# Kernel optimization log

Hardware: AMD Instinct MI355X
Metric: run time of the kernel (lower is better)

Reference implementation:

```python
import jax, jax.numpy as jnp
import numpy as np

NINF = -1e5  # large negative used for forbidden transitions (as in partial-tagger)


def setup_inputs() -> dict:
    key = jax.random.key(0)
    ks = jax.random.split(key, 10)
    B, T, H, N = 64, 512, 768, 25
    embeddings = jax.random.normal(ks[0], (B, T, H), jnp.float32)
    lengths = jax.random.randint(ks[1], (B,), T // 2, T + 1)
    mask = jnp.arange(T)[None, :] < lengths[:, None]  # [B,T] bool
    W = jax.random.normal(ks[2], (H, N), jnp.float32) / np.sqrt(H).astype(np.float32)
    b = jnp.zeros((N,), jnp.float32)
    transitions = jax.random.normal(ks[3], (N, N), jnp.float32) * 0.1
    start_transitions = jax.random.normal(ks[4], (N,), jnp.float32) * 0.1
    end_transitions = jax.random.normal(ks[5], (N,), jnp.float32) * 0.1
    start_constraints = (jax.random.uniform(ks[6], (N,)) < 0.7).at[0].set(True)
    end_constraints = (jax.random.uniform(ks[7], (N,)) < 0.7).at[0].set(True)
    transition_constraints = (jax.random.uniform(ks[8], (N, N)) < 0.6) | jnp.eye(N, dtype=bool)
    return dict(embeddings=embeddings, W=W, b=b, transitions=transitions,
                start_transitions=start_transitions, end_transitions=end_transitions,
                mask=mask, start_constraints=start_constraints, end_constraints=end_constraints,
                transition_constraints=transition_constraints, padding_index=0)


def _log_potentials(embeddings, W, b, transitions, start_transitions, end_transitions, mask):
    # emissions [B,T,N]; lp[b,t,k,j] = emit[b,t,j] + trans[k,j]
    B, T, _ = embeddings.shape
    N = transitions.shape[0]
    logits = jnp.einsum('bth,hn->btn', embeddings, W) + b
    lp = logits[:, :, None, :] + transitions[None, None]  # [B,T,N,N]
    first = jnp.broadcast_to((start_transitions + logits[:, 0])[:, None, :], (B, N, N))
    lp = lp.at[:, 0].set(first)
    last_pos = mask.sum(-1) - 1  # [B]
    end_mask = jnp.arange(T)[None, :] == last_pos[:, None]  # [B,T]
    lp = lp + jnp.where(end_mask[:, :, None, None], end_transitions[None, None, None, :], 0.0)
    return lp


def _constrain(lp, mask, start_constraints, end_constraints, transition_constraints):
    B, T, N, _ = lp.shape
    tc = jnp.where(transition_constraints, 0.0, NINF)  # [N,N]
    sc = jnp.where(start_constraints, 0.0, NINF)       # [N]
    ec = jnp.where(end_constraints, 0.0, NINF)         # [N]
    clp = lp + tc[None, None]
    clp = clp.at[:, 0].set(lp[:, 0] + sc[None, None, :])  # start constraint, no transition constraint at t=0
    last_pos = mask.sum(-1) - 1
    end_mask = jnp.arange(T)[None, :] == last_pos[:, None]
    clp = clp + jnp.where(end_mask[:, :, None, None], ec[None, None, None, :], 0.0)
    # padded steps: force a 0-score self transition so they don't affect the path score
    eye = jnp.where(jnp.eye(N, dtype=bool), 0.0, NINF)
    clp = jnp.where(mask[:, :, None, None], clp, eye[None, None])
    return clp


def _viterbi(clp):
    # clp: [B,T,N,N] constrained log potentials -> best tag sequence [B,T]
    clp_t = jnp.swapaxes(clp, 0, 1)  # time-major [T,B,N,N]
    alpha0 = clp_t[0, :, 0, :]  # first-step rows are identical -> take row 0, [B,N]

    def fwd_step(alpha, lp_t):
        scores = alpha[:, :, None] + lp_t  # [B,N,N]
        return jnp.max(scores, axis=1), jnp.argmax(scores, axis=1).astype(jnp.int32)

    alpha_T, backptrs = jax.lax.scan(fwd_step, alpha0, clp_t[1:])  # backptrs [T-1,B,N]
    last_tag = jnp.argmax(alpha_T, axis=-1).astype(jnp.int32)  # [B]

    def bwd_step(tag, bp):
        prev = jnp.take_along_axis(bp, tag[:, None], axis=1).squeeze(1)
        return prev, prev

    _, prevs = jax.lax.scan(bwd_step, last_tag, backptrs, reverse=True)  # [T-1,B]
    tags = jnp.concatenate([prevs, last_tag[None]], axis=0).T  # [B,T]
    return tags


def reference(embeddings, W, b, transitions, start_transitions, end_transitions,
              mask, start_constraints, end_constraints, transition_constraints, padding_index):
    lp = _log_potentials(embeddings, W, b, transitions, start_transitions, end_transitions, mask)
    clp = _constrain(lp, mask, start_constraints, end_constraints, transition_constraints)
    tags = _viterbi(clp)
    out_tags = tags * mask + padding_index * (~mask)
    return lp, out_tags
```

## Files before the change

### kernel.cpp

```cpp
#include <hip/hip_runtime.h>
#include <hip/hip_bf16.h>
#include <stdint.h>

#define NINF -100000.0f

constexpr int Bn = 64, Tn = 512, Hn = 768, Nn = 25;

typedef float float2v __attribute__((ext_vector_type(2)));

__device__ inline float2v pk_mul(float2v a, float2v b) {
    float2v d;
    asm("v_pk_mul_f32 %0, %1, %2" : "=v"(d) : "v"(a), "v"(b));
    return d;
}
__device__ inline float2v pk_add(float2v a, float2v b) {
    float2v d;
    asm("v_pk_add_f32 %0, %1, %2" : "=v"(d) : "v"(a), "v"(b));
    return d;
}

__device__ inline float ldf(const void* p, size_t i, bool isbf) {
    if (isbf) return __bfloat162float(((const __hip_bfloat16*)p)[i]);
    return ((const float*)p)[i];
}
__device__ inline int ldb(const void* p, int i, int bw) {
    if (bw == 1) return (int)((const uint8_t*)p)[i];
    if (bw == 8) return ((const int*)p)[2 * i];
    return ((const int*)p)[i];
}

__device__ inline float rdlane(float v, int lane) {
    return __int_as_float(__builtin_amdgcn_readlane(__float_as_int(v), lane));
}
__device__ inline int imin2(int a, int b) { return a < b ? a : b; }

__device__ inline float amax25(const float* s) {
    float a0 = fmaxf(fmaxf(s[0],  s[1]),  s[2]);
    float a1 = fmaxf(fmaxf(s[3],  s[4]),  s[5]);
    float a2 = fmaxf(fmaxf(s[6],  s[7]),  s[8]);
    float a3 = fmaxf(fmaxf(s[9],  s[10]), s[11]);
    float a4 = fmaxf(fmaxf(s[12], s[13]), s[14]);
    float a5 = fmaxf(fmaxf(s[15], s[16]), s[17]);
    float a6 = fmaxf(fmaxf(s[18], s[19]), s[20]);
    float a7 = fmaxf(fmaxf(s[21], s[22]), s[23]);
    float b0 = fmaxf(fmaxf(a0, a1), a2);
    float b1 = fmaxf(fmaxf(a3, a4), a5);
    float b2 = fmaxf(fmaxf(a6, a7), s[24]);
    return fmaxf(fmaxf(b0, b1), b2);
}

__device__ inline float stepx(float areg, float Lg, const float* ttc) {
    float s[25];
    {
#pragma clang fp contract(off)
#pragma unroll
        for (int k = 0; k < 25; k++) {
            float ak = rdlane(areg, k);
            s[k] = ak + (Lg + ttc[k]);
        }
    }
    return amax25(s);
}

__global__ __launch_bounds__(128) void k_front(
    const void* embv, const void* mask, const void* padidx,
    const void* W, const void* bv, const void* trans, const void* startt, const void* endt,
    const void* sc, const void* ec, const void* tc,
    int* flags, float* wstrans, float* wstc,
    float* wsstart, float* wsend, float* wsscm, float* wsecm,
    int* lengths, float* logitsF)
{
    __shared__ float etile[64][76];
    __shared__ float wtile[64][32];
    __shared__ float s_b[25];
    __shared__ int   s_isbf;
    __shared__ int   ws2[2];

    int tid = threadIdx.x;
    int bid = blockIdx.x;

    if (tid < 64) {
        const uint16_t* e16 = (const uint16_t*)embv;
        uint16_t v = e16[tid];
        int ex = (v >> 7) & 0xFF;
        bool sane = (ex >= 100 && ex <= 140);
        unsigned long long ball = __ballot(sane);
        if (tid == 0) s_isbf = (__popcll(ball) >= 56) ? 1 : 0;
    }
    __syncthreads();
    bool isbf = s_isbf != 0;

    if (bid >= 512) {
        int pb = bid - 512;
        const int* mw = (const int*)mask;
        int w0 = mw[0], w1 = mw[1];
        int bw;
        if ((unsigned)w0 > 1u) bw = 1;
        else if (w0 == 1 && w1 == 0) bw = 8;
        else bw = 4;
        if (pb == 0 && tid == 0) {
            flags[0] = isbf ? 1 : 0;
            flags[1] = bw;
            flags[2] = ((const int*)padidx)[0];
        }
        {
            int s = 0;
#pragma unroll
            for (int u = 0; u < 4; u++)
                s += (ldb(mask, pb * Tn + u * 128 + tid, bw) ? 1 : 0);
            for (int off = 32; off; off >>= 1) s += __shfl_down(s, off, 64);
            if ((tid & 63) == 0) ws2[tid >> 6] = s;
            __syncthreads();
            if (tid == 0) lengths[pb] = ws2[0] + ws2[1];
        }
        int gid = pb * 128 + tid;
        int gsz = 64 * 128;
        for (int i = gid; i < Nn; i += gsz) {
            wsstart[i] = ldf(startt, i, isbf);
            wsend[i]   = ldf(endt, i, isbf);
            wsscm[i]   = ldb(sc, i, bw) ? 0.0f : NINF;
            wsecm[i]   = ldb(ec, i, bw) ? 0.0f : NINF;
        }
        for (int i = gid; i < Nn * Nn; i += gsz) {
            wstrans[i] = ldf(trans, i, isbf);
            wstc[i]    = ldb(tc, i, bw) ? 0.0f : NINF;
        }
        return;
    }

    int r    = tid >> 1;
    int half = tid & 1;
    int j0   = half ? 12 : 0;
    int row0 = bid * 64;
    int row  = row0 + r;

    if (tid < 25) s_b[tid] = ldf(bv, tid, isbf);

    float2v acc2[6];
#pragma unroll
    for (int k = 0; k < 6; k++) acc2[k] = (float2v){0.0f, 0.0f};
    float acc12 = 0.0f;

    for (int c = 0; c < 12; c++) {
        __syncthreads();
        if (isbf) {
            const uint16_t* ep = (const uint16_t*)embv;
#pragma unroll
            for (int it = 0; it < 8; it++) {
                int idx = it * 128 + tid;
                int rr = idx >> 4;
                int q  = idx & 15;
                const ushort4* p4 = (const ushort4*)(ep + (size_t)(row0 + rr) * Hn + c * 64);
                ushort4 u = p4[q];
                float4 f;
                f.x = __bfloat162float(*(const __hip_bfloat16*)&u.x);
                f.y = __bfloat162float(*(const __hip_bfloat16*)&u.y);
                f.z = __bfloat162float(*(const __hip_bfloat16*)&u.z);
                f.w = __bfloat162float(*(const __hip_bfloat16*)&u.w);
                *(float4*)&etile[rr][q * 4] = f;
            }
        } else {
            const float* ep = (const float*)embv;
#pragma unroll
            for (int it = 0; it < 8; it++) {
                int idx = it * 128 + tid;
                int rr = idx >> 4;
                int q  = idx & 15;
                const float4* p4 = (const float4*)(ep + (size_t)(row0 + rr) * Hn + c * 64);
                *(float4*)&etile[rr][q * 4] = p4[q];
            }
        }
        for (int i = tid; i < 1600; i += 128) {
            int hh = i / 25, jj = i - hh * 25;
            wtile[hh][jj] = ldf(W, (size_t)c * 1600 + i, isbf);
        }
        __syncthreads();
        {
#pragma clang fp contract(off)
            for (int h4 = 0; h4 < 16; h4++) {
                float4 e4 = *(const float4*)&etile[r][h4 * 4];
#pragma unroll
                for (int u = 0; u < 4; u++) {
                    int hh = h4 * 4 + u;
                    float e = (u == 0) ? e4.x : (u == 1) ? e4.y : (u == 2) ? e4.z : e4.w;
                    float2v ee = (float2v){e, e};
                    const float4* wp = (const float4*)&wtile[hh][j0];
                    float4 w0 = wp[0];
                    float4 w1 = wp[1];
                    float4 w2 = wp[2];
                    float  wl = wtile[hh][j0 + 12];
                    acc2[0] = pk_add(acc2[0], pk_mul(ee, (float2v){w0.x, w0.y}));
                    acc2[1] = pk_add(acc2[1], pk_mul(ee, (float2v){w0.z, w0.w}));
                    acc2[2] = pk_add(acc2[2], pk_mul(ee, (float2v){w1.x, w1.y}));
                    acc2[3] = pk_add(acc2[3], pk_mul(ee, (float2v){w1.z, w1.w}));
                    acc2[4] = pk_add(acc2[4], pk_mul(ee, (float2v){w2.x, w2.y}));
                    acc2[5] = pk_add(acc2[5], pk_mul(ee, (float2v){w2.z, w2.w}));
                    acc12 = acc12 + e * wl;
                }
            }
        }
    }

    {
#pragma clang fp contract(off)
#pragma unroll
        for (int p = 0; p < 6; p++) {
            int j = j0 + 2 * p;
            logitsF[(size_t)row * 25 + j]     = acc2[p][0] + s_b[j];
            logitsF[(size_t)row * 25 + j + 1] = acc2[p][1] + s_b[j + 1];
        }
        if (half) logitsF[(size_t)row * 25 + 24] = acc12 + s_b[24];
    }
}

struct SharedV {
    float   lgl[Tn * Nn];
    float   alpha[Tn][26];
    uint8_t bp[511][32];
    uint8_t tags[512];
};
struct SharedL {
    float s_trans[625];
    float s_start[25];
    float s_end[25];
};

__global__ __launch_bounds__(512) void k_tail(
    const float* logitsF, const float* wstrans, const float* wstc,
    const float* wsstart, const float* wsend, const float* wsscm, const float* wsecm,
    const int* lengths, const int* flags, void* out)
{
    __shared__ union { SharedV v; SharedL l; } smem;
    int tid = threadIdx.x;
    bool isbf = flags[0] != 0;

    if (blockIdx.x >= 64) {
        for (int i = tid; i < 625; i += 512) smem.l.s_trans[i] = wstrans[i];
        if (tid < 25) { smem.l.s_start[tid] = wsstart[tid]; smem.l.s_end[tid] = wsend[tid]; }
        __syncthreads();

        int rw0 = (blockIdx.x - 64) * 16;
        int b = rw0 >> 9;
        int last = lengths[b] - 1;
        const float* lg0 = logitsF + (size_t)rw0 * 25;
        size_t obase = (size_t)rw0 * 625;

        for (int idx = tid; idx < 16 * 625; idx += 512) {
            int rr = idx / 625;
            int e  = idx - rr * 625;
            int j  = e % 25;
            int t  = (rw0 + rr) & 511;
            float lg = lg0[rr * 25 + j];
            float v;
            {
#pragma clang fp contract(off)
                if (t == 0) v = smem.l.s_start[j] + lg;
                else        v = lg + smem.l.s_trans[e];
                if (t == last) v += smem.l.s_end[j];
            }
            size_t o = obase + idx;
            if (isbf) ((__hip_bfloat16*)out)[o] = __float2bfloat16(v);
            else      ((float*)out)[o] = v;
        }
        return;
    }

    int b  = blockIdx.x;
    int len  = lengths[b];
    int last = len - 1;
    int padv = flags[2];
    int L   = tid & 63;
    int wid = tid >> 6;
    bool act = (L < 25);
    int j = act ? L : 0;

    {
        const float4* src = (const float4*)(logitsF + (size_t)b * (Tn * Nn));
        float4* dst = (float4*)smem.v.lgl;
        for (int i = tid; i < (Tn * Nn) / 4; i += 512) dst[i] = src[i];
    }

    float tcol[25], tccol[25], ttc[25];
#pragma unroll
    for (int k = 0; k < 25; k++) {
        tcol[k]  = wstrans[k * 25 + j];
        tccol[k] = wstc[k * 25 + j];
        ttc[k] = tcol[k] + tccol[k];
    }
    float endj = wsend[j];
    float ecmj = wsecm[j];

    __syncthreads();

    float areg = 0.0f;
    if (wid == 0) {
        {
#pragma clang fp contract(off)
            areg = (wsstart[j] + smem.v.lgl[j]) + wsscm[j];
        }
        if (act) smem.v.alpha[0][L] = areg;

        int tEndX = last - 1;
        int t = 1;
        for (; t + 7 <= tEndX; t += 8) {
            float Lg8[8];
#pragma unroll
            for (int u = 0; u < 8; u++) Lg8[u] = smem.v.lgl[(t + u) * 25 + j];
            float a8[8];
#pragma unroll
            for (int u = 0; u < 8; u++) { areg = stepx(areg, Lg8[u], ttc); a8[u] = areg; }
            if (act) {
#pragma unroll
                for (int u = 0; u < 8; u++) smem.v.alpha[t + u][L] = a8[u];
            }
        }
        for (; t <= tEndX; ++t) {
            float Lg = smem.v.lgl[t * 25 + j];
            areg = stepx(areg, Lg, ttc);
            if (act) smem.v.alpha[t][L] = areg;
        }
        {
            float Lg = smem.v.lgl[last * 25 + j];
            float s[25];
            {
#pragma clang fp contract(off)
#pragma unroll
                for (int k = 0; k < 25; k++) {
                    float ak = rdlane(areg, k);
                    float v = (((Lg + tcol[k]) + endj) + tccol[k]) + ecmj;
                    s[k] = ak + v;
                }
            }
            areg = amax25(s);
            if (act) smem.v.alpha[last][L] = areg;
        }
    }
    __syncthreads();

    for (int t = 1 + wid; t <= last; t += 8) {
        float ap = smem.v.alpha[t - 1][j];
        float mj = smem.v.alpha[t][j];
        float Lg = smem.v.lgl[t * 25 + j];

        float s[25];
        if (t < last) {
#pragma clang fp contract(off)
#pragma unroll
            for (int k = 0; k < 25; k++) {
                float ak = rdlane(ap, k);
                s[k] = ak + (Lg + ttc[k]);
            }
        } else {
#pragma clang fp contract(off)
#pragma unroll
            for (int k = 0; k < 25; k++) {
                float ak = rdlane(ap, k);
                float v = (((Lg + tcol[k]) + endj) + tccol[k]) + ecmj;
                s[k] = ak + v;
            }
        }

        int ik[25];
#pragma unroll
        for (int k = 0; k < 25; k++) ik[k] = (s[k] == mj) ? k : 32;
        int q0 = imin2(imin2(ik[0],  ik[1]),  ik[2]);
        int q1 = imin2(imin2(ik[3],  ik[4]),  ik[5]);
        int q2 = imin2(imin2(ik[6],  ik[7]),  ik[8]);
        int q3 = imin2(imin2(ik[9],  ik[10]), ik[11]);
        int q4 = imin2(imin2(ik[12], ik[13]), ik[14]);
        int q5 = imin2(imin2(ik[15], ik[16]), ik[17]);
        int q6 = imin2(imin2(ik[18], ik[19]), ik[20]);
        int q7 = imin2(imin2(ik[21], ik[22]), ik[23]);
        int r0 = imin2(imin2(q0, q1), q2);
        int r1 = imin2(imin2(q3, q4), q5);
        int r2 = imin2(imin2(q6, q7), ik[24]);
        int mi = imin2(imin2(r0, r1), r2);

        if (act) smem.v.bp[t - 1][L] = (uint8_t)mi;
    }
    __syncthreads();

    if (wid == 0) {
        float am = rdlane(areg, 0);
        int ami = 0;
#pragma unroll
        for (int k = 1; k < 25; k++) {
            float v2 = rdlane(areg, k);
            bool g = v2 > am;
            am  = g ? v2 : am;
            ami = g ? k  : ami;
        }
        int tag = ami;
        if (L == 0) smem.v.tags[last] = (uint8_t)tag;

        int Lc = L & 31;
        int k2 = last - 1;
        while (k2 >= 7) {
            int c0 = smem.v.bp[k2    ][Lc];
            int c1 = smem.v.bp[k2 - 1][Lc];
            int c2 = smem.v.bp[k2 - 2][Lc];
            int c3 = smem.v.bp[k2 - 3][Lc];
            int c4 = smem.v.bp[k2 - 4][Lc];
            int c5 = smem.v.bp[k2 - 5][Lc];
            int c6 = smem.v.bp[k2 - 6][Lc];
            int c7 = smem.v.bp[k2 - 7][Lc];
            tag = __builtin_amdgcn_readlane(c0, tag); if (L == 0) smem.v.tags[k2    ] = (uint8_t)tag;
            tag = __builtin_amdgcn_readlane(c1, tag); if (L == 0) smem.v.tags[k2 - 1] = (uint8_t)tag;
            tag = __builtin_amdgcn_readlane(c2, tag); if (L == 0) smem.v.tags[k2 - 2] = (uint8_t)tag;
            tag = __builtin_amdgcn_readlane(c3, tag); if (L == 0) smem.v.tags[k2 - 3] = (uint8_t)tag;
            tag = __builtin_amdgcn_readlane(c4, tag); if (L == 0) smem.v.tags[k2 - 4] = (uint8_t)tag;
            tag = __builtin_amdgcn_readlane(c5, tag); if (L == 0) smem.v.tags[k2 - 5] = (uint8_t)tag;
            tag = __builtin_amdgcn_readlane(c6, tag); if (L == 0) smem.v.tags[k2 - 6] = (uint8_t)tag;
            tag = __builtin_amdgcn_readlane(c7, tag); if (L == 0) smem.v.tags[k2 - 7] = (uint8_t)tag;
            k2 -= 8;
        }
        while (k2 >= 0) {
            int c = smem.v.bp[k2][Lc];
            tag = __builtin_amdgcn_readlane(c, tag);
            if (L == 0) smem.v.tags[k2] = (uint8_t)tag;
            k2--;
        }
    }
    __syncthreads();

    size_t base = 20480000ull;
    {
        int t = tid;
        float val = (t < len) ? (float)smem.v.tags[t] : (float)padv;
        size_t o = base + (size_t)b * 512 + t;
        if (isbf) ((__hip_bfloat16*)out)[o] = __float2bfloat16(val);
        else      ((float*)out)[o] = val;
    }
}

extern "C" void kernel_launch(void* const* d_in, const int* in_sizes, int n_in,
                              void* d_out, int out_size, void* d_ws, size_t ws_size,
                              hipStream_t stream) {
    const void* emb  = d_in[0];
    const void* W    = d_in[1];
    const void* bv   = d_in[2];
    const void* tr   = d_in[3];
    const void* st   = d_in[4];
    const void* en   = d_in[5];
    const void* mask = d_in[6];
    const void* sc   = d_in[7];
    const void* ec   = d_in[8];
    const void* tc   = d_in[9];
    const void* pad  = d_in[10];

    char* ws = (char*)d_ws;
    int*    flags    = (int*)ws;
    int*    lengths  = (int*)(ws + 64);
    float*  wsstart  = (float*)(ws + 512);
    float*  wsend    = (float*)(ws + 640);
    float*  wsscm    = (float*)(ws + 768);
    float*  wsecm    = (float*)(ws + 896);
    float*  wstrans  = (float*)(ws + 1024);
    float*  wstc     = (float*)(ws + 3584);
    float*  logitsF  = (float*)(ws + 82944);

    k_front<<<576, 128, 0, stream>>>(emb, mask, pad, W, bv, tr, st, en, sc, ec, tc,
                                     flags, wstrans, wstc, wsstart, wsend, wsscm, wsecm,
                                     lengths, logitsF);
    k_tail<<<2112, 512, 0, stream>>>(logitsF, wstrans, wstc, wsstart, wsend,
                                     wsscm, wsecm, lengths, flags, d_out);
}
```

Baseline: 419.1 us.

## Split front kernel into prep and GEMM kernels with full W resident in LDS

The fused front kernel is split into a small prep kernel (flags, lengths, constraint tables) and a dedicated GEMM kernel. The GEMM kernel stages the whole 768x25 weight matrix in LDS once per block and streams each embedding row straight from global memory into registers, with double-buffered prefetch on the bf16 path. This removes the per-chunk LDS staging of embeddings and the twelve barrier pairs. In the tail kernel, the end-step transition and constraint columns are reloaded from memory instead of being held in registers, which lowers register pressure. The trade-offs are an extra kernel launch, about 86KB of LDS per block limiting occupancy to a single block, and uncoalesced per-thread row reads of embeddings.

```diff
diff --git a/kernel.cpp b/kernel.cpp
--- a/kernel.cpp
+++ b/kernel.cpp
@@ -7,6 +7,7 @@
 constexpr int Bn = 64, Tn = 512, Hn = 768, Nn = 25;
 
 typedef float float2v __attribute__((ext_vector_type(2)));
+typedef unsigned short ushortv8 __attribute__((ext_vector_type(8)));
 
 __device__ inline float2v pk_mul(float2v a, float2v b) {
     float2v d;
@@ -27,6 +28,9 @@
     if (bw == 1) return (int)((const uint8_t*)p)[i];
     if (bw == 8) return ((const int*)p)[2 * i];
     return ((const int*)p)[i];
+}
+__device__ inline float bf2f(uint16_t h) {
+    return __bfloat162float(*(const __hip_bfloat16*)&h);
 }
 
 __device__ inline float rdlane(float v, int lane) {
@@ -62,22 +66,77 @@
     return amax25(s);
 }
 
-__global__ __launch_bounds__(128) void k_front(
-    const void* embv, const void* mask, const void* padidx,
-    const void* W, const void* bv, const void* trans, const void* startt, const void* endt,
+__global__ __launch_bounds__(256) void k_prep(
+    const void* emb, const void* mask, const void* padidx,
+    const void* trans, const void* startt, const void* endt,
     const void* sc, const void* ec, const void* tc,
-    int* flags, float* wstrans, float* wstc,
-    float* wsstart, float* wsend, float* wsscm, float* wsecm,
-    int* lengths, float* logitsF)
+    int* flags, float* wsstart, float* wsend, float* wsscm, float* wsecm,
+    float* wstrans, float* wstc, int* lengths)
 {
-    __shared__ float etile[64][76];
-    __shared__ float wtile[64][32];
+    __shared__ int s_isbf, s_bw;
+    __shared__ int ws4[4];
+    int blk = blockIdx.x;
+    int tid = threadIdx.x;
+
+    if (tid < 64) {
+        const uint16_t* e16 = (const uint16_t*)emb;
+        uint16_t v = e16[tid];
+        int ex = (v >> 7) & 0xFF;
+        bool sane = (ex >= 100 && ex <= 140);
+        unsigned long long ball = __ballot(sane);
+        int cnt = __popcll(ball);
+        if (tid == 0) {
+            int isbf = (cnt >= 56) ? 1 : 0;
+            const int* mw = (const int*)mask;
+            int w0 = mw[0];
+            int w1 = mw[1];
+            int bw;
+            if ((unsigned)w0 > 1u) bw = 1;
+            else if (w0 == 1 && w1 == 0) bw = 8;
+            else bw = 4;
+            s_isbf = isbf; s_bw = bw;
+            if (blk == 0) {
+                flags[0] = isbf;
+                flags[1] = bw;
+                flags[2] = ((const int*)padidx)[0];
+            }
+        }
+    }
+    __syncthreads();
+    bool isbf = s_isbf != 0;
+    int bw = s_bw;
+
+    {
+        int s = (ldb(mask, blk * Tn + tid, bw) ? 1 : 0)
+              + (ldb(mask, blk * Tn + 256 + tid, bw) ? 1 : 0);
+        for (int off = 32; off; off >>= 1) s += __shfl_down(s, off, 64);
+        if ((tid & 63) == 0) ws4[tid >> 6] = s;
+        __syncthreads();
+        if (tid == 0) lengths[blk] = ws4[0] + ws4[1] + ws4[2] + ws4[3];
+    }
+
+    int gid = blk * 256 + tid;
+    int gsz = 64 * 256;
+    for (int i = gid; i < Nn; i += gsz) {
+        wsstart[i] = ldf(startt, i, isbf);
+        wsend[i]   = ldf(endt, i, isbf);
+        wsscm[i]   = ldb(sc, i, bw) ? 0.0f : NINF;
+        wsecm[i]   = ldb(ec, i, bw) ? 0.0f : NINF;
+    }
+    for (int i = gid; i < Nn * Nn; i += gsz) {
+        wstrans[i] = ldf(trans, i, isbf);
+        wstc[i]    = ldb(tc, i, bw) ? 0.0f : NINF;
+    }
+}
+
+__global__ __launch_bounds__(256) void k_gemm(
+    const void* embv, const void* W, const void* bv, float* logitsF)
+{
+    __shared__ float wall[768 * 28];
     __shared__ float s_b[25];
     __shared__ int   s_isbf;
-    __shared__ int   ws2[2];
 
     int tid = threadIdx.x;
-    int bid = blockIdx.x;
 
     if (tid < 64) {
         const uint16_t* e16 = (const uint16_t*)embv;
@@ -90,112 +149,111 @@
     __syncthreads();
     bool isbf = s_isbf != 0;
 
-    if (bid >= 512) {
-        int pb = bid - 512;
-        const int* mw = (const int*)mask;
-        int w0 = mw[0], w1 = mw[1];
-        int bw;
-        if ((unsigned)w0 > 1u) bw = 1;
-        else if (w0 == 1 && w1 == 0) bw = 8;
-        else bw = 4;
-        if (pb == 0 && tid == 0) {
-            flags[0] = isbf ? 1 : 0;
-            flags[1] = bw;
-            flags[2] = ((const int*)padidx)[0];
-        }
-        {
-            int s = 0;
-#pragma unroll
-            for (int u = 0; u < 4; u++)
-                s += (ldb(mask, pb * Tn + u * 128 + tid, bw) ? 1 : 0);
-            for (int off = 32; off; off >>= 1) s += __shfl_down(s, off, 64);
-            if ((tid & 63) == 0) ws2[tid >> 6] = s;
-            __syncthreads();
-            if (tid == 0) lengths[pb] = ws2[0] + ws2[1];
-        }
-        int gid = pb * 128 + tid;
-        int gsz = 64 * 128;
-        for (int i = gid; i < Nn; i += gsz) {
-            wsstart[i] = ldf(startt, i, isbf);
-            wsend[i]   = ldf(endt, i, isbf);
-            wsscm[i]   = ldb(sc, i, bw) ? 0.0f : NINF;
-            wsecm[i]   = ldb(ec, i, bw) ? 0.0f : NINF;
-        }
-        for (int i = gid; i < Nn * Nn; i += gsz) {
-            wstrans[i] = ldf(trans, i, isbf);
-            wstc[i]    = ldb(tc, i, bw) ? 0.0f : NINF;
-        }
-        return;
-    }
+    if (isbf) {
+        const ushortv8* wp = (const ushortv8*)W;
+        for (int k = tid; k < 2400; k += 256) {
+            ushortv8 u = wp[k];
+            int base = k * 8;
+#pragma unroll
+            for (int uu = 0; uu < 8; uu++) {
+                int e = base + uu;
+                int hh = e / 25, jj = e - hh * 25;
+                wall[hh * 28 + jj] = bf2f(u[uu]);
+            }
+        }
+    } else {
+        const float4* wp = (const float4*)W;
+        for (int k = tid; k < 4800; k += 256) {
+            float4 f = wp[k];
+            int base = k * 4;
+#pragma unroll
+            for (int uu = 0; uu < 4; uu++) {
+                int e = base + uu;
+                int hh = e / 25, jj = e - hh * 25;
+                float v = (uu == 0) ? f.x : (uu == 1) ? f.y : (uu == 2) ? f.z : f.w;
+                wall[hh * 28 + jj] = v;
+            }
+        }
+    }
+    if (tid < 25) s_b[tid] = ldf(bv, tid, isbf);
+    __syncthreads();
 
     int r    = tid >> 1;
     int half = tid & 1;
     int j0   = half ? 12 : 0;
-    int row0 = bid * 64;
-    int row  = row0 + r;
-
-    if (tid < 25) s_b[tid] = ldf(bv, tid, isbf);
+    int row  = blockIdx.x * 128 + r;
 
     float2v acc2[6];
 #pragma unroll
     for (int k = 0; k < 6; k++) acc2[k] = (float2v){0.0f, 0.0f};
     float acc12 = 0.0f;
 
-    for (int c = 0; c < 12; c++) {
-        __syncthreads();
-        if (isbf) {
-            const uint16_t* ep = (const uint16_t*)embv;
-#pragma unroll
-            for (int it = 0; it < 8; it++) {
-                int idx = it * 128 + tid;
-                int rr = idx >> 4;
-                int q  = idx & 15;
-                const ushort4* p4 = (const ushort4*)(ep + (size_t)(row0 + rr) * Hn + c * 64);
-                ushort4 u = p4[q];
-                float4 f;
-                f.x = __bfloat162float(*(const __hip_bfloat16*)&u.x);
-                f.y = __bfloat162float(*(const __hip_bfloat16*)&u.y);
-                f.z = __bfloat162float(*(const __hip_bfloat16*)&u.z);
-                f.w = __bfloat162float(*(const __hip_bfloat16*)&u.w);
-                *(float4*)&etile[rr][q * 4] = f;
-            }
-        } else {
-            const float* ep = (const float*)embv;
-#pragma unroll
-            for (int it = 0; it < 8; it++) {
-                int idx = it * 128 + tid;
-                int rr = idx >> 4;
-                int q  = idx & 15;
-                const float4* p4 = (const float4*)(ep + (size_t)(row0 + rr) * Hn + c * 64);
-                *(float4*)&etile[rr][q * 4] = p4[q];
-            }
-        }
-        for (int i = tid; i < 1600; i += 128) {
-            int hh = i / 25, jj = i - hh * 25;
-            wtile[hh][jj] = ldf(W, (size_t)c * 1600 + i, isbf);
-        }
-        __syncthreads();
-        {
-#pragma clang fp contract(off)
-            for (int h4 = 0; h4 < 16; h4++) {
-                float4 e4 = *(const float4*)&etile[r][h4 * 4];
-#pragma unroll
-                for (int u = 0; u < 4; u++) {
-                    int hh = h4 * 4 + u;
-                    float e = (u == 0) ? e4.x : (u == 1) ? e4.y : (u == 2) ? e4.z : e4.w;
-                    float2v ee = (float2v){e, e};
-                    const float4* wp = (const float4*)&wtile[hh][j0];
-                    float4 w0 = wp[0];
-                    float4 w1 = wp[1];
-                    float4 w2 = wp[2];
-                    float  wl = wtile[hh][j0 + 12];
-                    acc2[0] = pk_add(acc2[0], pk_mul(ee, (float2v){w0.x, w0.y}));
-                    acc2[1] = pk_add(acc2[1], pk_mul(ee, (float2v){w0.z, w0.w}));
-                    acc2[2] = pk_add(acc2[2], pk_mul(ee, (float2v){w1.x, w1.y}));
-                    acc2[3] = pk_add(acc2[3], pk_mul(ee, (float2v){w1.z, w1.w}));
-                    acc2[4] = pk_add(acc2[4], pk_mul(ee, (float2v){w2.x, w2.y}));
-                    acc2[5] = pk_add(acc2[5], pk_mul(ee, (float2v){w2.z, w2.w}));
-                    acc12 = acc12 + e * wl;
+    if (isbf) {
+        const ushortv8* ep = (const ushortv8*)((const uint16_t*)embv + (size_t)row * Hn);
+        ushortv8 eA[8], eB[8];
+#pragma unroll
+        for (int g = 0; g < 8; g++) eA[g] = ep[g];
+        for (int c = 0; c < 12; c++) {
+            if (c < 11) {
+#pragma unroll
+                for (int g = 0; g < 8; g++) eB[g] = ep[(c + 1) * 8 + g];
+            }
+            {
+#pragma clang fp contract(off)
+#pragma unroll
+                for (int g = 0; g < 8; g++) {
+#pragma unroll
+                    for (int u = 0; u < 8; u++) {
+                        int hg = c * 64 + g * 8 + u;
+                        float e = bf2f(eA[g][u]);
+                        float2v ee = (float2v){e, e};
+                        const float4* wp4 = (const float4*)&wall[hg * 28 + j0];
+                        float4 w0 = wp4[0];
+                        float4 w1 = wp4[1];
+                        float4 w2 = wp4[2];
+                        float  wl = wall[hg * 28 + j0 + 12];
+                        acc2[0] = pk_add(acc2[0], pk_mul(ee, (float2v){w0.x, w0.y}));
+                        acc2[1] = pk_add(acc2[1], pk_mul(ee, (float2v){w0.z, w0.w}));
+                        acc2[2] = pk_add(acc2[2], pk_mul(ee, (float2v){w1.x, w1.y}));
+                        acc2[3] = pk_add(acc2[3], pk_mul(ee, (float2v){w1.z, w1.w}));
+                        acc2[4] = pk_add(acc2[4], pk_mul(ee, (float2v){w2.x, w2.y}));
+                        acc2[5] = pk_add(acc2[5], pk_mul(ee, (float2v){w2.z, w2.w}));
+                        acc12 = acc12 + e * wl;
+                    }
+                }
+            }
+#pragma unroll
+            for (int g = 0; g < 8; g++) eA[g] = eB[g];
+        }
+    } else {
+        const float4* ep = (const float4*)((const float*)embv + (size_t)row * Hn);
+        for (int c = 0; c < 12; c++) {
+            float4 cur[16];
+#pragma unroll
+            for (int g = 0; g < 16; g++) cur[g] = ep[c * 16 + g];
+            {
+#pragma clang fp contract(off)
+#pragma unroll
+                for (int g = 0; g < 16; g++) {
+#pragma unroll
+                    for (int u = 0; u < 4; u++) {
+                        int hg = c * 64 + g * 4 + u;
+                        float e = (u == 0) ? cur[g].x : (u == 1) ? cur[g].y
+                                : (u == 2) ? cur[g].z : cur[g].w;
+                        float2v ee = (float2v){e, e};
+                        const float4* wp4 = (const float4*)&wall[hg * 28 + j0];
+                        float4 w0 = wp4[0];
+                        float4 w1 = wp4[1];
+                        float4 w2 = wp4[2];
+                        float  wl = wall[hg * 28 + j0 + 12];
+                        acc2[0] = pk_add(acc2[0], pk_mul(ee, (float2v){w0.x, w0.y}));
+                        acc2[1] = pk_add(acc2[1], pk_mul(ee, (float2v){w0.z, w0.w}));
+                        acc2[2] = pk_add(acc2[2], pk_mul(ee, (float2v){w1.x, w1.y}));
+                        acc2[3] = pk_add(acc2[3], pk_mul(ee, (float2v){w1.z, w1.w}));
+                        acc2[4] = pk_add(acc2[4], pk_mul(ee, (float2v){w2.x, w2.y}));
+                        acc2[5] = pk_add(acc2[5], pk_mul(ee, (float2v){w2.z, w2.w}));
+                        acc12 = acc12 + e * wl;
+                    }
                 }
             }
         }
@@ -280,12 +338,10 @@
         for (int i = tid; i < (Tn * Nn) / 4; i += 512) dst[i] = src[i];
     }
 
-    float tcol[25], tccol[25], ttc[25];
+    float ttc[25];
 #pragma unroll
     for (int k = 0; k < 25; k++) {
-        tcol[k]  = wstrans[k * 25 + j];
-        tccol[k] = wstc[k * 25 + j];
-        ttc[k] = tcol[k] + tccol[k];
+        ttc[k] = wstrans[k * 25 + j] + wstc[k * 25 + j];
     }
     float endj = wsend[j];
     float ecmj = wsecm[j];
@@ -326,8 +382,10 @@
 #pragma clang fp contract(off)
 #pragma unroll
                 for (int k = 0; k < 25; k++) {
+                    float tr = wstrans[k * 25 + j];
+                    float tv = wstc[k * 25 + j];
                     float ak = rdlane(areg, k);
-                    float v = (((Lg + tcol[k]) + endj) + tccol[k]) + ecmj;
+                    float v = (((Lg + tr) + endj) + tv) + ecmj;
                     s[k] = ak + v;
                 }
             }
@@ -354,8 +412,10 @@
 #pragma clang fp contract(off)
 #pragma unroll
             for (int k = 0; k < 25; k++) {
+                float tr = wstrans[k * 25 + j];
+                float tv = wstc[k * 25 + j];
                 float ak = rdlane(ap, k);
-                float v = (((Lg + tcol[k]) + endj) + tccol[k]) + ecmj;
+                float v = (((Lg + tr) + endj) + tv) + ecmj;
                 s[k] = ak + v;
             }
         }
@@ -459,9 +519,10 @@
     float*  wstc     = (float*)(ws + 3584);
     float*  logitsF  = (float*)(ws + 82944);
 
-    k_front<<<576, 128, 0, stream>>>(emb, mask, pad, W, bv, tr, st, en, sc, ec, tc,
-                                     flags, wstrans, wstc, wsstart, wsend, wsscm, wsecm,
-                                     lengths, logitsF);
+    k_prep<<<64, 256, 0, stream>>>(emb, mask, pad, tr, st, en, sc, ec, tc,
+                                   flags, wsstart, wsend, wsscm, wsecm,
+                                   wstrans, wstc, lengths);
+    k_gemm<<<256, 256, 0, stream>>>(emb, W, bv, logitsF);
     k_tail<<<2112, 512, 0, stream>>>(logitsF, wstrans, wstc, wsstart, wsend,
                                      wsscm, wsecm, lengths, flags, d_out);
 }
```

New measurement: 373.2 us. 10.9% less time.
